# Optimization experiments

Hardware: AMD Instinct MI355X
Metric: run time of the kernel (lower is better)

Reference implementation:

```python
import jax, jax.numpy as jnp
import numpy as np

LAM = 0.003  # kernel_lam squash threshold


def setup_inputs() -> dict:
    key = jax.random.key(0)
    k1, k2, k3, k4 = jax.random.split(key, 4)
    B, L, H, Lk = 2, 4096, 2048, 128
    u = jax.random.normal(k1, (B, L, H), jnp.float32)
    # LongConvKernel parameter [channels=1, H, Lk]; scaled so squash keeps most taps nonzero
    kernel = jax.random.normal(k2, (1, H, Lk), jnp.float32) * 0.05
    D = jax.random.normal(k3, (1, H), jnp.float32)  # skip term [channels, H]
    # output_linear: nn.Linear(H, 2H) followed by GLU(dim=-1)
    W = jax.random.normal(k4, (2 * H, H), jnp.float32) / np.sqrt(H)
    b = jnp.zeros((2 * H,), jnp.float32)
    return {"u": u, "kernel": kernel, "D": D, "W": W, "b": b}


def reference(u, kernel, D, W, b):
    # u: [B, L, H] -> transpose to [B, H, L]
    B, L, H = u.shape
    ut = jnp.transpose(u, (0, 2, 1)).astype(jnp.float32)  # bhl
    # LongConvKernel forward: squash k = relu(|k| - lam) * sign(k)
    k = jnp.maximum(jnp.abs(kernel) - LAM, 0.0) * jnp.sign(kernel)  # [C, H, Lk]
    Lk = kernel.shape[-1]
    n = Lk + L  # FFT size for linear (causal) convolution
    k_f = jnp.fft.rfft(k, n=n)          # [C, H, n//2+1]
    u_f = jnp.fft.rfft(ut, n=n)         # [B, H, n//2+1]
    y_f = jnp.einsum('bhl,chl->bchl', u_f, k_f)
    y = jnp.fft.irfft(y_f, n=n)[..., :L]  # [B, C, H, L]
    # source adds the D skip term twice (duplicated line) -> factor 2
    y = y + 2.0 * jnp.einsum('bhl,ch->bchl', ut, D)
    # rearrange 'b c h l -> b (c h) l' then transpose -> [B, L, C*H]
    y = jnp.transpose(y.reshape(B, -1, L), (0, 2, 1))
    y = jax.nn.gelu(y, approximate=False)  # torch GELU is exact erf
    z = y @ W.T + b                     # [B, L, 2H]
    a, g = jnp.split(z, 2, axis=-1)     # GLU along last dim
    return a * jax.nn.sigmoid(g)        # [B, L, H]
```

## Files before the change

kernel.cpp:

```cpp
#include <hip/hip_runtime.h>
#include <hip/hip_bf16.h>
#include <cstdint>

constexpr int Bc  = 2;
constexpr int Lc  = 4096;
constexpr int Hc  = 2048;
constexpr int LKc = 128;
constexpr float LAMc = 0.003f;

typedef __attribute__((ext_vector_type(8))) __bf16 bf16x8;
typedef __attribute__((ext_vector_type(4))) float  f32x4;
typedef __attribute__((ext_vector_type(8))) unsigned short ushort8;

__device__ __forceinline__ unsigned short f2bf_bits(float v) {
  union { __hip_bfloat16 b; unsigned short u; } cv;
  cv.b = __float2bfloat16(v);
  return cv.u;
}
__device__ __forceinline__ float bf_bits2f(unsigned short u) {
  union { unsigned int i; float f; } cv;
  cv.i = ((unsigned int)u) << 16;
  return cv.f;
}

__device__ __forceinline__ void gl_lds16(const void* g, void* lds) {
  __builtin_amdgcn_global_load_lds(
      (const __attribute__((address_space(1))) uint32_t*)(uintptr_t)g,
      (__attribute__((address_space(3))) uint32_t*)(uint32_t)(uintptr_t)lds,
      16, 0, 0);
}

__global__ __launch_bounds__(256) void tapfrag_kernel(
    const float* __restrict__ kin, unsigned short* __restrict__ Afr) {
  const int idx  = blockIdx.x * 256 + threadIdx.x;
  const int lane = idx & 63;
  const int idx2 = idx >> 6;
  const int h  = idx2 / 5;
  const int cc = idx2 - h * 5;
  const int m = lane & 15, quad = lane >> 4;
  const int jb = m + 32 * cc - 32 + 8 * quad;
  ushort8 o;
#pragma unroll
  for (int jj = 0; jj < 8; ++jj) {
    const int j = jb + jj;
    float v = 0.f;
    if (j >= 0 && j < LKc) {
      const float x = kin[h * LKc + j];
      const float a = fabsf(x) - LAMc;
      v = (a > 0.f) ? copysignf(a, x) : 0.f;
    }
    o[jj] = f2bf_bits(v);
  }
  ((ushort8*)Afr)[idx] = o;
}

__global__ __launch_bounds__(256) void wcast_kernel(
    const float* __restrict__ W, __hip_bfloat16* __restrict__ Wb) {
  const int idx = (blockIdx.x * 256 + threadIdx.x) * 4;
  const float4 v = *(const float4*)(W + idx);
  Wb[idx + 0] = __float2bfloat16(v.x);
  Wb[idx + 1] = __float2bfloat16(v.y);
  Wb[idx + 2] = __float2bfloat16(v.z);
  Wb[idx + 3] = __float2bfloat16(v.w);
}

__global__ __launch_bounds__(256) void conv_mfma_kernel(
    const float* __restrict__ u, const unsigned short* __restrict__ Afr,
    const float* __restrict__ Dp, unsigned short* __restrict__ Am) {
  __shared__ __align__(16) unsigned short ur[16 * 664];
  __shared__ __align__(16) unsigned short ot[512 * 17];

  const int t    = threadIdx.x;
  const int lane = t & 63;
  const int wv   = t >> 6;
  const int l16  = lane & 15;
  const int quad = lane >> 4;
  const int l0 = blockIdx.x * 512;
  const int h0 = blockIdx.y * 16;
  const int b  = blockIdx.z;

  const size_t ubase = (size_t)b * Lc * Hc + h0;

#pragma unroll 4
  for (int i = 0; i < 41; ++i) {
    const int e  = (i << 8) + t;
    const int hl = e & 15;
    const int x  = e >> 4;
    const int l  = l0 + 528 - x;
    float v = 0.f;
    if (l >= 0) v = u[ubase + (size_t)min(l, Lc - 1) * Hc + hl];
    ur[hl * 664 + x] = f2bf_bits(v);
  }
  __syncthreads();

#pragma unroll 1
  for (int hi = 0; hi < 4; ++hi) {
    const int hl = (wv << 2) | hi;
    const int h  = h0 + hl;
    bf16x8 af[5];
    const unsigned short* afp = Afr + ((size_t)(h * 5) * 64 + lane) * 8;
#pragma unroll
    for (int cc = 0; cc < 5; ++cc) af[cc] = *(const bf16x8*)(afp + cc * 512);
    const float dv = 2.f * Dp[h];
    const unsigned short* urh = &ur[hl * 664];
#pragma unroll
    for (int nt = 0; nt < 2; ++nt) {
      f32x4 acc = f32x4{0.f, 0.f, 0.f, 0.f};
      const int bbase = 496 - 256 * nt - 16 * l16 + 8 * quad;
#pragma unroll
      for (int cc = 0; cc < 5; ++cc) {
        const bf16x8 bf = *(const bf16x8*)(urh + bbase + 32 * cc);
        acc = __builtin_amdgcn_mfma_f32_16x16x32_bf16(af[cc], bf, acc, 0, 0, 0);
      }
#pragma unroll
      for (int r = 0; r < 4; ++r) {
        const int lc = quad * 4 + r + 16 * l16;
        const float uu = bf_bits2f(urh[528 - 256 * nt - lc]);
        const float y = fmaf(dv, uu, acc[r]);
        const float g = 0.5f * y * (1.f + erff(y * 0.70710678118654752f));
        ot[(nt * 256 + lc) * 17 + hl] = f2bf_bits(g);
      }
    }
  }
  __syncthreads();

#pragma unroll
  for (int rr = 0; rr < 2; ++rr) {
    const int lc = (rr << 8) + t;
    const unsigned short* row = &ot[lc * 17];
    unsigned int w[8];
#pragma unroll
    for (int p = 0; p < 8; ++p)
      w[p] = (unsigned int)row[2 * p] | ((unsigned int)row[2 * p + 1] << 16);
    unsigned short* dst = Am + ((size_t)(b * Lc + l0 + lc)) * Hc + h0;
    *(uint4*)(dst)     = make_uint4(w[0], w[1], w[2], w[3]);
    *(uint4*)(dst + 8) = make_uint4(w[4], w[5], w[6], w[7]);
  }
}

__global__ __launch_bounds__(256, 2) void gemm_glu_kernel(
    const __hip_bfloat16* __restrict__ A, const __hip_bfloat16* __restrict__ Wb,
    const float* __restrict__ bias, float* __restrict__ out) {
  __shared__ __align__(16) __hip_bfloat16 As[128 * 32];
  __shared__ __align__(16) __hip_bfloat16 Bs[128 * 32];

  const int t    = threadIdx.x;
  const int lane = t & 63;
  const int wv   = t >> 6;
  const int quad = lane >> 4;
  const int l16  = lane & 15;
  const int m0 = blockIdx.x * 128;
  const int n0 = blockIdx.y * 64;

  f32x4 accA[2][4], accG[2][4];
#pragma unroll
  for (int i = 0; i < 2; ++i)
#pragma unroll
    for (int j = 0; j < 4; ++j) {
      accA[i][j] = f32x4{0.f, 0.f, 0.f, 0.f};
      accG[i][j] = f32x4{0.f, 0.f, 0.f, 0.f};
    }

  const int srow = t >> 2;
  const int scol = (t & 3) * 8;
  const __hip_bfloat16* gA0 = A  + (size_t)(m0 + srow) * Hc + scol;
  const __hip_bfloat16* gA1 = A  + (size_t)(m0 + 64 + srow) * Hc + scol;
  const __hip_bfloat16* gBa = Wb + (size_t)(n0 + srow) * Hc + scol;
  const __hip_bfloat16* gBg = Wb + (size_t)(Hc + n0 + srow) * Hc + scol;
  char* ldsA0 = (char*)As + wv * 1024;
  char* ldsA1 = (char*)As + 4096 + wv * 1024;
  char* ldsBa = (char*)Bs + wv * 1024;
  char* ldsBg = (char*)Bs + 4096 + wv * 1024;

  const bf16x8* ar0 = (const bf16x8*)(As + (wv * 32 + l16) * 32 + quad * 8);
  const bf16x8* ar1 = (const bf16x8*)(As + (wv * 32 + 16 + l16) * 32 + quad * 8);

  for (int it = 0; it < 64; ++it) {
    const int k0 = it * 32;
    gl_lds16(gA0 + k0, ldsA0);
    gl_lds16(gA1 + k0, ldsA1);
    gl_lds16(gBa + k0, ldsBa);
    gl_lds16(gBg + k0, ldsBg);
    __syncthreads();
    const bf16x8 af0 = *ar0;
    const bf16x8 af1 = *ar1;
#pragma unroll
    for (int nj = 0; nj < 4; ++nj) {
      const bf16x8 ba = *(const bf16x8*)(Bs + (nj * 16 + l16) * 32 + quad * 8);
      const bf16x8 bg = *(const bf16x8*)(Bs + (64 + nj * 16 + l16) * 32 + quad * 8);
      accA[0][nj] = __builtin_amdgcn_mfma_f32_16x16x32_bf16(af0, ba, accA[0][nj], 0, 0, 0);
      accA[1][nj] = __builtin_amdgcn_mfma_f32_16x16x32_bf16(af1, ba, accA[1][nj], 0, 0, 0);
      accG[0][nj] = __builtin_amdgcn_mfma_f32_16x16x32_bf16(af0, bg, accG[0][nj], 0, 0, 0);
      accG[1][nj] = __builtin_amdgcn_mfma_f32_16x16x32_bf16(af1, bg, accG[1][nj], 0, 0, 0);
    }
    __syncthreads();
  }

  const int mbase = m0 + wv * 32;
#pragma unroll
  for (int mi = 0; mi < 2; ++mi) {
#pragma unroll
    for (int nj = 0; nj < 4; ++nj) {
      const int n = n0 + nj * 16 + l16;
      const float ba_ = bias[n];
      const float bg_ = bias[Hc + n];
#pragma unroll
      for (int r = 0; r < 4; ++r) {
        const int m = mbase + mi * 16 + quad * 4 + r;
        const float a = accA[mi][nj][r] + ba_;
        const float g = accG[mi][nj][r] + bg_;
        out[(size_t)m * Hc + n] = a * (1.f / (1.f + expf(-g)));
      }
    }
  }
}

extern "C" void kernel_launch(void* const* d_in, const int* in_sizes, int n_in,
                              void* d_out, int out_size, void* d_ws, size_t ws_size,
                              hipStream_t stream) {
  const float* u    = (const float*)d_in[0];
  const float* kin  = (const float*)d_in[1];
  const float* Dp   = (const float*)d_in[2];
  const float* W    = (const float*)d_in[3];
  const float* bias = (const float*)d_in[4];
  float* out = (float*)d_out;

  char* ws = (char*)d_ws;
  unsigned short* Afr = (unsigned short*)ws;
  __hip_bfloat16* Wb  = (__hip_bfloat16*)ws;
  unsigned short* Am  = (unsigned short*)(ws + (16 << 20));

  tapfrag_kernel<<<(Hc * 5 * 64) / 256, 256, 0, stream>>>(kin, Afr);
  conv_mfma_kernel<<<dim3(Lc / 512, Hc / 16, Bc), 256, 0, stream>>>(u, Afr, Dp, Am);
  wcast_kernel<<<(2 * Hc * Hc) / 1024, 256, 0, stream>>>(W, Wb);
  gemm_glu_kernel<<<dim3((Bc * Lc) / 128, Hc / 64), 256, 0, stream>>>(
      (const __hip_bfloat16*)Am, Wb, bias, out);
}
```

Baseline: 377.4 us.

## Rewrite GLU GEMM with 256x256 tiles, 4-stage LDS pipeline and swizzled grid

The GEMM+GLU kernel now uses 512-thread blocks computing 256 rows by 128 value plus 128 gate columns. It stages K tiles through a 4-slot LDS ring (128 KB), prefetching two tiles ahead with global_load_lds, and places explicit waitcnt, barriers and setprio around the MFMA bursts. Block IDs are remapped so neighbouring blocks share W/A tiles in cache. The aim is higher arithmetic intensity per LDS byte and hiding global latency, compared with the old single-buffered 128x128 tile that synchronised twice per K step. In exchange it uses much more LDS and registers per block, which lowers occupancy, and correctness depends on hand-placed waitcnt counts.

```diff
diff --git a/kernel.cpp b/kernel.cpp
--- a/kernel.cpp
+++ b/kernel.cpp
@@ -138,78 +138,113 @@
   }
 }
 
-__global__ __launch_bounds__(256, 2) void gemm_glu_kernel(
+constexpr int KTILES = Hc / 32;
+
+__global__ __launch_bounds__(512, 2) void gemm_glu_kernel(
     const __hip_bfloat16* __restrict__ A, const __hip_bfloat16* __restrict__ Wb,
     const float* __restrict__ bias, float* __restrict__ out) {
-  __shared__ __align__(16) __hip_bfloat16 As[128 * 32];
-  __shared__ __align__(16) __hip_bfloat16 Bs[128 * 32];
+  __shared__ __align__(16) char lds[131072];
 
   const int t    = threadIdx.x;
   const int lane = t & 63;
-  const int wv   = t >> 6;
+  const int w    = t >> 6;
+  const int l16  = lane & 15;
   const int quad = lane >> 4;
-  const int l16  = lane & 15;
-  const int m0 = blockIdx.x * 128;
-  const int n0 = blockIdx.y * 64;
-
-  f32x4 accA[2][4], accG[2][4];
-#pragma unroll
-  for (int i = 0; i < 2; ++i)
-#pragma unroll
-    for (int j = 0; j < 4; ++j) {
-      accA[i][j] = f32x4{0.f, 0.f, 0.f, 0.f};
-      accG[i][j] = f32x4{0.f, 0.f, 0.f, 0.f};
-    }
-
-  const int srow = t >> 2;
-  const int scol = (t & 3) * 8;
-  const __hip_bfloat16* gA0 = A  + (size_t)(m0 + srow) * Hc + scol;
-  const __hip_bfloat16* gA1 = A  + (size_t)(m0 + 64 + srow) * Hc + scol;
-  const __hip_bfloat16* gBa = Wb + (size_t)(n0 + srow) * Hc + scol;
-  const __hip_bfloat16* gBg = Wb + (size_t)(Hc + n0 + srow) * Hc + scol;
-  char* ldsA0 = (char*)As + wv * 1024;
-  char* ldsA1 = (char*)As + 4096 + wv * 1024;
-  char* ldsBa = (char*)Bs + wv * 1024;
-  char* ldsBg = (char*)Bs + 4096 + wv * 1024;
-
-  const bf16x8* ar0 = (const bf16x8*)(As + (wv * 32 + l16) * 32 + quad * 8);
-  const bf16x8* ar1 = (const bf16x8*)(As + (wv * 32 + 16 + l16) * 32 + quad * 8);
-
-  for (int it = 0; it < 64; ++it) {
-    const int k0 = it * 32;
-    gl_lds16(gA0 + k0, ldsA0);
-    gl_lds16(gA1 + k0, ldsA1);
-    gl_lds16(gBa + k0, ldsBa);
-    gl_lds16(gBg + k0, ldsBg);
-    __syncthreads();
-    const bf16x8 af0 = *ar0;
-    const bf16x8 af1 = *ar1;
-#pragma unroll
-    for (int nj = 0; nj < 4; ++nj) {
-      const bf16x8 ba = *(const bf16x8*)(Bs + (nj * 16 + l16) * 32 + quad * 8);
-      const bf16x8 bg = *(const bf16x8*)(Bs + (64 + nj * 16 + l16) * 32 + quad * 8);
-      accA[0][nj] = __builtin_amdgcn_mfma_f32_16x16x32_bf16(af0, ba, accA[0][nj], 0, 0, 0);
-      accA[1][nj] = __builtin_amdgcn_mfma_f32_16x16x32_bf16(af1, ba, accA[1][nj], 0, 0, 0);
-      accG[0][nj] = __builtin_amdgcn_mfma_f32_16x16x32_bf16(af0, bg, accG[0][nj], 0, 0, 0);
-      accG[1][nj] = __builtin_amdgcn_mfma_f32_16x16x32_bf16(af1, bg, accG[1][nj], 0, 0, 0);
-    }
-    __syncthreads();
-  }
-
-  const int mbase = m0 + wv * 32;
-#pragma unroll
-  for (int mi = 0; mi < 2; ++mi) {
-#pragma unroll
-    for (int nj = 0; nj < 4; ++nj) {
-      const int n = n0 + nj * 16 + l16;
-      const float ba_ = bias[n];
-      const float bg_ = bias[Hc + n];
+  const int wr   = w >> 2;
+  const int wc   = w & 3;
+
+  const int bid = blockIdx.x;
+  const int wg  = (bid & 7) * 64 + (bid >> 3);
+  const int m0g = (wg & 31) * 256;
+  const int n0  = (wg >> 5) * 128;
+
+  const __hip_bfloat16* gsrc[4];
+#pragma unroll
+  for (int u = 0; u < 2; ++u) {
+    const int f = u * 8 + w;
+    gsrc[u] = A + (size_t)(m0g + f * 16 + l16) * Hc + quad * 8;
+    const int wrow = ((f >> 1) & 1) * Hc + n0 + (f >> 2) * 32 + (f & 1) * 16 + l16;
+    gsrc[2 + u] = Wb + (size_t)wrow * Hc + quad * 8;
+  }
+
+  f32x4 acc[8][4];
+#pragma unroll
+  for (int i = 0; i < 8; ++i)
+#pragma unroll
+    for (int j = 0; j < 4; ++j) acc[i][j] = f32x4{0.f, 0.f, 0.f, 0.f};
+
+#define STAGE(tile, idx)                                                      \
+  gl_lds16(gsrc[idx] + (size_t)(tile) * 32,                                   \
+           lds + ((tile) & 3) * 32768 + (((idx) >> 1) & 1) * 16384 +          \
+               (((idx) & 1) * 8 + w) * 1024)
+
+#pragma unroll
+  for (int i = 0; i < 4; ++i) STAGE(0, i);
+#pragma unroll
+  for (int i = 0; i < 4; ++i) STAGE(1, i);
+  asm volatile("s_waitcnt vmcnt(4)" ::: "memory");
+  __builtin_amdgcn_s_barrier();
+
+  const char* sAbase = lds + wr * 8192 + lane * 16;
+  const char* sBbase = lds + 16384 + wc * 4096 + lane * 16;
+
+#pragma unroll 2
+  for (int kt = 0; kt < KTILES; ++kt) {
+    const int slot = (kt & 3) * 32768;
+    const char* sA = sAbase + slot;
+    const char* sB = sBbase + slot;
+    bf16x8 afr[4], bfr[4];
+
+#pragma unroll
+    for (int i = 0; i < 4; ++i) afr[i] = *(const bf16x8*)(sA + i * 1024);
+#pragma unroll
+    for (int i = 0; i < 4; ++i) bfr[i] = *(const bf16x8*)(sB + i * 1024);
+    if (kt + 2 < KTILES) { STAGE(kt + 2, 0); STAGE(kt + 2, 1); }
+    __builtin_amdgcn_s_barrier();
+    asm volatile("s_waitcnt lgkmcnt(0)" ::: "memory");
+    __builtin_amdgcn_s_setprio(1);
+#pragma unroll
+    for (int mf = 0; mf < 4; ++mf)
+#pragma unroll
+      for (int nf = 0; nf < 4; ++nf)
+        acc[mf][nf] = __builtin_amdgcn_mfma_f32_16x16x32_bf16(
+            afr[mf], bfr[nf], acc[mf][nf], 0, 0, 0);
+    __builtin_amdgcn_s_setprio(0);
+    __builtin_amdgcn_s_barrier();
+
+#pragma unroll
+    for (int i = 0; i < 4; ++i) afr[i] = *(const bf16x8*)(sA + (4 + i) * 1024);
+    if (kt + 2 < KTILES) { STAGE(kt + 2, 2); STAGE(kt + 2, 3); }
+    __builtin_amdgcn_s_barrier();
+    asm volatile("s_waitcnt lgkmcnt(0)" ::: "memory");
+    __builtin_amdgcn_s_setprio(1);
+#pragma unroll
+    for (int mf = 0; mf < 4; ++mf)
+#pragma unroll
+      for (int nf = 0; nf < 4; ++nf)
+        acc[4 + mf][nf] = __builtin_amdgcn_mfma_f32_16x16x32_bf16(
+            afr[mf], bfr[nf], acc[4 + mf][nf], 0, 0, 0);
+    __builtin_amdgcn_s_setprio(0);
+    if (kt < KTILES - 2) asm volatile("s_waitcnt vmcnt(4)" ::: "memory");
+    else                 asm volatile("s_waitcnt vmcnt(0)" ::: "memory");
+    __builtin_amdgcn_s_barrier();
+  }
+#undef STAGE
+
+  const int mwb = m0g + wr * 128 + quad * 4;
+  const int nb  = n0 + wc * 32 + l16;
+#pragma unroll
+  for (int j = 0; j < 2; ++j) {
+    const int n = nb + j * 16;
+    const float ba = bias[n];
+    const float bg = bias[Hc + n];
+#pragma unroll
+    for (int mf = 0; mf < 8; ++mf) {
 #pragma unroll
       for (int r = 0; r < 4; ++r) {
-        const int m = mbase + mi * 16 + quad * 4 + r;
-        const float a = accA[mi][nj][r] + ba_;
-        const float g = accG[mi][nj][r] + bg_;
-        out[(size_t)m * Hc + n] = a * (1.f / (1.f + expf(-g)));
+        const float a = acc[mf][j][r] + ba;
+        const float g = acc[mf][j + 2][r] + bg;
+        out[(size_t)(mwb + mf * 16 + r) * Hc + n] = a * (1.f / (1.f + expf(-g)));
       }
     }
   }
@@ -233,6 +268,6 @@
   tapfrag_kernel<<<(Hc * 5 * 64) / 256, 256, 0, stream>>>(kin, Afr);
   conv_mfma_kernel<<<dim3(Lc / 512, Hc / 16, Bc), 256, 0, stream>>>(u, Afr, Dp, Am);
   wcast_kernel<<<(2 * Hc * Hc) / 1024, 256, 0, stream>>>(W, Wb);
-  gemm_glu_kernel<<<dim3((Bc * Lc) / 128, Hc / 64), 256, 0, stream>>>(
+  gemm_glu_kernel<<<dim3((Bc * Lc / 256) * (Hc / 128)), 512, 0, stream>>>(
       (const __hip_bfloat16*)Am, Wb, bias, out);
 }
```

After: 362.9 us. 3.8% less time.
